# Kernel tuning notes

Hardware: AMD Instinct MI355X
Metric: run time of the kernel (lower is better)

Reference implementation:

```python
import jax, jax.numpy as jnp
import numpy as np
from jax import lax

N_NODES = 10000
IN_DIM = 144
OUT_DIM = 700
THETA_DIM = 256
TOP_K = 5
BN_EPS = 1e-5
LRELU_SLOPE = 0.01


def setup_inputs() -> dict:
    key = jax.random.key(0)
    ks = jax.random.split(key, 5)
    return {
        "H": jax.random.normal(ks[0], (N_NODES, IN_DIM), dtype=jnp.float32),
        "bn_gamma": jnp.ones((IN_DIM,), jnp.float32),
        "bn_beta": jnp.zeros((IN_DIM,), jnp.float32),
        "W_theta": jax.random.normal(ks[1], (IN_DIM, THETA_DIM), jnp.float32) * (1.0 / np.sqrt(IN_DIM)),
        "b_theta": jax.random.normal(ks[2], (THETA_DIM,), jnp.float32) * 0.01,
        "W_out": jax.random.normal(ks[3], (IN_DIM, OUT_DIM), jnp.float32) * (1.0 / np.sqrt(IN_DIM)),
        "b_out": jax.random.normal(ks[4], (OUT_DIM,), jnp.float32) * 0.01,
    }


def _forward(H, bn_gamma, bn_beta, W_theta, b_theta, W_out, b_out):
    # BatchNorm1d over nodes (training-mode batch statistics, biased variance)
    mean = H.mean(axis=0)
    var = ((H - mean) ** 2).mean(axis=0)
    Hn = (H - mean) * lax.rsqrt(var + BN_EPS) * bn_gamma + bn_beta

    # theta projection -> SAM (spectral angle) adjacency; torch code detaches here
    Hx = Hn @ W_theta + b_theta                                  # [n, 256]
    Xn = Hx / jnp.maximum(jnp.linalg.norm(Hx, axis=1, keepdims=True), 1e-12)
    cos = jnp.clip(Xn @ Xn.T, -1.0, 1.0)                         # [n, n]
    sam = jnp.nan_to_num(jnp.arccos(cos))
    A = jnp.clip(jax.nn.sigmoid(jnp.exp(-0.2 * sam)), 0.1, None)
    A = lax.stop_gradient(A)  # SAM() goes through .detach() in torch

    # per-row top-k=5 mask (argsort(-A) first k columns)
    _, idx = lax.top_k(A, TOP_K)                                  # [n, k]
    n = A.shape[0]
    mask = jnp.zeros_like(A).at[jnp.arange(n)[:, None], idx].set(1.0)
    A = A * mask

    # symmetric normalization D^-0.5 A D^-0.5 (diagonal mm as row/col scaling)
    d = A.sum(axis=1) ** -0.5                                     # [n]
    A_hat = A * d[:, None] * d[None, :]

    out = A_hat @ (Hn @ W_out + b_out)                            # [n, out_dim]
    out = jnp.where(out >= 0, out, LRELU_SLOPE * out)             # LeakyReLU
    return out, A


def reference(H, bn_gamma, bn_beta, W_theta, b_theta, W_out, b_out):
    return _forward(H, bn_gamma, bn_beta, W_theta, b_theta, W_out, b_out)
```

## Files before the change

### kernel.cpp

```cpp
#include <hip/hip_runtime.h>
#include <hip/hip_bf16.h>
#include <math.h>

#define N_NODES 10000
#define NPAD2   10240
#define IN_DIM  144
#define TD      256
#define OD      700
#define TOPK    5
#define GK      160
#define GLD     168
#define LDT     72

typedef __attribute__((ext_vector_type(8))) short short8v;
typedef __attribute__((ext_vector_type(4))) float f32x4;

__device__ inline unsigned short f32_to_bf16_rne(float f){
    unsigned int u = __float_as_uint(f);
    unsigned int r = u + 0x7fffu + ((u >> 16) & 1u);
    return (unsigned short)(r >> 16);
}

__global__ void bn_partial(const float* __restrict__ H, double* __restrict__ part){
    int c = threadIdx.x;
    int b = blockIdx.x;
    if (c >= IN_DIM) return;
    int r0 = b * 80;
    double s = 0.0, q = 0.0;
    #pragma unroll 4
    for (int r = r0; r < r0 + 80; ++r){
        double v = (double)H[r*IN_DIM + c];
        s += v; q += v*v;
    }
    part[b*288 + c]       = s;
    part[b*288 + 144 + c] = q;
}

__global__ void bn_finish(const double* __restrict__ part, double* __restrict__ stats){
    int c = threadIdx.x;
    if (c >= 288) return;
    double s = 0.0;
    for (int b = 0; b < 125; ++b) s += part[b*288 + c];
    stats[c] = s;
}

__global__ __launch_bounds__(256) void theta_kernel(
    const float* __restrict__ H, const float* __restrict__ gam, const float* __restrict__ bet,
    const float* __restrict__ Wt, const float* __restrict__ bt, const double* __restrict__ stats,
    const float* __restrict__ Wo, unsigned short* __restrict__ WoT16,
    float* __restrict__ Xn32, unsigned short* __restrict__ Xh, unsigned short* __restrict__ Hn16)
{
    __shared__ double hn[4][IN_DIM];
    __shared__ double red[4][4];
    __shared__ double invs[4];
    int tid = threadIdx.x;
    int r0 = blockIdx.x * 4;

    if (blockIdx.x < 704 && tid < GK){
        int jj = blockIdx.x;
        float v = (jj < OD && tid < IN_DIM) ? Wo[tid*OD + jj] : 0.0f;
        WoT16[(size_t)jj*GK + tid] = f32_to_bf16_rne(v);
    }

    if (tid < GK){
        int c = tid;
        bool real = (c < IN_DIM);
        double mean = 0.0, scale = 0.0, bb = 0.0;
        if (real){
            mean  = stats[c] * (1.0/10000.0);
            double var = stats[144+c] * (1.0/10000.0) - mean*mean;
            scale = (1.0/sqrt(var + 1e-5)) * (double)gam[c];
            bb    = (double)bet[c];
        }
        for (int r = 0; r < 4; ++r){
            int row = r0 + r;
            float vf = 0.0f;
            if (real && row < N_NODES)
                vf = (float)(((double)H[row*IN_DIM + c] - mean)*scale + bb);
            if (row < 10048) Hn16[(size_t)row*GK + c] = f32_to_bf16_rne(vf);
            if (real) hn[r][c] = (double)vf;
        }
    }
    __syncthreads();

    int j = tid;
    double a0,a1,a2,a3;
    a0=a1=a2=a3=(double)bt[j];
    for (int k = 0; k < IN_DIM; ++k){
        double w = (double)Wt[k*TD + j];
        a0 += hn[0][k]*w; a1 += hn[1][k]*w; a2 += hn[2][k]*w; a3 += hn[3][k]*w;
    }
    float hx0=(float)a0, hx1=(float)a1, hx2=(float)a2, hx3=(float)a3;
    double n0=(double)hx0*(double)hx0, n1=(double)hx1*(double)hx1,
           n2=(double)hx2*(double)hx2, n3=(double)hx3*(double)hx3;
    #pragma unroll
    for (int off=32; off>0; off>>=1){
        n0 += __shfl_down(n0, off);
        n1 += __shfl_down(n1, off);
        n2 += __shfl_down(n2, off);
        n3 += __shfl_down(n3, off);
    }
    int lane = tid & 63, wave = tid >> 6;
    if (lane == 0){ red[0][wave]=n0; red[1][wave]=n1; red[2][wave]=n2; red[3][wave]=n3; }
    __syncthreads();
    if (tid < 4){
        double s = red[tid][0]+red[tid][1]+red[tid][2]+red[tid][3];
        invs[tid] = 1.0 / fmax(sqrt(s), 1e-12);
    }
    __syncthreads();

    float hx[4] = {hx0,hx1,hx2,hx3};
    #pragma unroll
    for (int r = 0; r < 4; ++r){
        int row = r0 + r;
        float xn = 0.0f;
        if (row < N_NODES) xn = (float)((double)hx[r]*invs[r]);
        Xn32[(size_t)row*TD + j] = xn;
        Xh  [(size_t)row*TD + j] = f32_to_bf16_rne(xn);
    }
}

__global__ __launch_bounds__(256,2) void gproj(const unsigned short* __restrict__ Hn16,
    const unsigned short* __restrict__ WoT16, const float* __restrict__ bo,
    float* __restrict__ G)
{
    __shared__ short Al[64*GLD];
    __shared__ short Wl[2][64*GLD];
    int tid = threadIdx.x;
    int w = tid >> 6, lane = tid & 63;
    int l15 = lane & 15, l4 = lane >> 4;
    int i0 = blockIdx.x * 64;

    int sr = tid >> 2, sc = tid & 3;
    #pragma unroll
    for (int p = 0; p < 5; ++p){
        int cb = sc + (p<<2);
        *(short8v*)(&Al[sr*GLD + cb*8]) =
            *(const short8v*)(&Hn16[(size_t)(i0+sr)*GK + cb*8]);
    }
    #pragma unroll
    for (int p = 0; p < 5; ++p){
        int cb = sc + (p<<2);
        *(short8v*)(&Wl[0][sr*GLD + cb*8]) =
            *(const short8v*)(&WoT16[(size_t)sr*GK + cb*8]);
    }
    __syncthreads();

    for (int jt = 0; jt < 11; ++jt){
        int cur = jt & 1;
        bool pf = (jt < 10);
        short8v g[5];
        if (pf){
            #pragma unroll
            for (int p = 0; p < 5; ++p){
                int cb = sc + (p<<2);
                g[p] = *(const short8v*)(&WoT16[(size_t)((jt+1)*64 + sr)*GK + cb*8]);
            }
        }
        f32x4 acc[4];
        #pragma unroll
        for (int n=0;n<4;++n) acc[n] = (f32x4){0.f,0.f,0.f,0.f};
        #pragma unroll
        for (int ks = 0; ks < 5; ++ks){
            short8v af = *(const short8v*)(&Al[(w*16 + l15)*GLD + ks*32 + l4*8]);
            #pragma unroll
            for (int n=0;n<4;++n){
                short8v bf = *(const short8v*)(&Wl[cur][(n*16 + l15)*GLD + ks*32 + l4*8]);
                acc[n] = __builtin_amdgcn_mfma_f32_16x16x32_bf16(af, bf, acc[n], 0, 0, 0);
            }
        }
        #pragma unroll
        for (int n=0;n<4;++n){
            int jcol = jt*64 + n*16 + l15;
            if (jcol < OD){
                float b = bo[jcol];
                #pragma unroll
                for (int q=0;q<4;++q){
                    int irow = i0 + w*16 + l4*4 + q;
                    if (irow < N_NODES)
                        G[(size_t)irow*OD + jcol] = acc[n][q] + b;
                }
            }
        }
        if (pf){
            #pragma unroll
            for (int p = 0; p < 5; ++p){
                int cb = sc + (p<<2);
                *(short8v*)(&Wl[cur^1][sr*GLD + cb*8]) = g[p];
            }
        }
        __syncthreads();
    }
}

__global__ __launch_bounds__(256,3) void cos_blk(const unsigned short* __restrict__ Xh,
                                                 unsigned int* __restrict__ pkey)
{
    __shared__ unsigned int smem[10240];
    short* Al = (short*)smem;
    short* Bl = ((short*)smem) + 128*LDT;

    int t = blockIdx.x;
    int bi = 0, rem = t;
    while (rem >= 80 - bi){ rem -= 80 - bi; ++bi; }
    int bj = bi + rem;
    int i0 = bi * 128;
    int j0 = bj * 128;

    int tid = threadIdx.x;
    int w = tid >> 6, lane = tid & 63;
    int l15 = lane & 15, l4 = lane >> 4;

    f32x4 acc[2][8];
    #pragma unroll
    for (int jf=0;jf<2;++jf){
        #pragma unroll
        for (int f=0;f<8;++f) acc[jf][f] = (f32x4){0.f,0.f,0.f,0.f};
    }

    int str = tid >> 3;
    int scb = tid & 7;

    for (int kc = 0; kc < TD; kc += 64){
        __syncthreads();
        #pragma unroll
        for (int p=0;p<4;++p){
            int r = p*32 + str;
            *(short8v*)(&Al[r*LDT + scb*8]) =
                *(const short8v*)(&Xh[(size_t)(i0+r)*TD + kc + scb*8]);
            *(short8v*)(&Bl[r*LDT + scb*8]) =
                *(const short8v*)(&Xh[(size_t)(j0+r)*TD + kc + scb*8]);
        }
        __syncthreads();
        #pragma unroll
        for (int ks=0; ks<2; ++ks){
            short8v af0 = *(const short8v*)(&Bl[(w*32 +  0 + l15)*LDT + ks*32 + l4*8]);
            short8v af1 = *(const short8v*)(&Bl[(w*32 + 16 + l15)*LDT + ks*32 + l4*8]);
            #pragma unroll
            for (int f=0; f<8; ++f){
                short8v bf = *(const short8v*)(&Al[(f*16 + l15)*LDT + ks*32 + l4*8]);
                acc[0][f] = __builtin_amdgcn_mfma_f32_16x16x32_bf16(af0, bf, acc[0][f], 0,0,0);
                acc[1][f] = __builtin_amdgcn_mfma_f32_16x16x32_bf16(af1, bf, acc[1][f], 0,0,0);
            }
        }
    }
    __syncthreads();

    unsigned int* lists = smem;

    #pragma unroll
    for (int f=0; f<8; ++f){
        unsigned int t5[5] = {0u,0u,0u,0u,0u};
        #pragma unroll
        for (int jf=0; jf<2; ++jf){
            #pragma unroll
            for (int q=0; q<4; ++q){
                float v = acc[jf][f][q];
                int jl = w*32 + jf*16 + l4*4 + q;
                unsigned int u = __float_as_uint(v);
                unsigned int key = ((int)u < 0) ? ~u : (u | 0x80000000u);
                unsigned int pk = (key & 0xFFFFFF80u) | (unsigned int)(127 - jl);
                if (pk > t5[4]){
                    t5[4] = pk;
                    #pragma unroll
                    for (int s=4;s>0;--s){
                        if (t5[s] > t5[s-1]){ unsigned int tp=t5[s]; t5[s]=t5[s-1]; t5[s-1]=tp; }
                    }
                }
            }
        }
        int row  = f*16 + l15;
        int base = row*80 + (w*4 + l4)*5;
        #pragma unroll
        for (int s=0;s<5;++s) lists[base+s] = t5[s];
    }
    __syncthreads();

    if (tid < 128){
        unsigned int b5[5] = {0u,0u,0u,0u,0u};
        int rb = tid*80;
        for (int c=0;c<80;++c){
            unsigned int pk = lists[rb + c];
            if (pk > b5[4]){
                b5[4] = pk;
                #pragma unroll
                for (int s=4;s>0;--s){
                    if (b5[s] > b5[s-1]){ unsigned int tp=b5[s]; b5[s]=b5[s-1]; b5[s-1]=tp; }
                }
            }
        }
        size_t gb = (size_t)(i0 + tid)*400 + (size_t)bj*5;
        #pragma unroll
        for (int s=0;s<5;++s) pkey[gb + s] = b5[s];
    }

    if (bi == bj) return;

    __syncthreads();

    #pragma unroll
    for (int jf=0; jf<2; ++jf){
        #pragma unroll
        for (int q=0; q<4; ++q){
            unsigned int t5[5] = {0u,0u,0u,0u,0u};
            #pragma unroll
            for (int f=0; f<8; ++f){
                float v = acc[jf][f][q];
                int il = f*16 + l15;
                unsigned int u = __float_as_uint(v);
                unsigned int key = ((int)u < 0) ? ~u : (u | 0x80000000u);
                unsigned int pk = (key & 0xFFFFFF80u) | (unsigned int)(127 - il);
                if (pk > t5[4]){
                    t5[4] = pk;
                    #pragma unroll
                    for (int s=4;s>0;--s){
                        if (t5[s] > t5[s-1]){ unsigned int tp=t5[s]; t5[s]=t5[s-1]; t5[s-1]=tp; }
                    }
                }
            }
            int jl   = w*32 + jf*16 + l4*4 + q;
            int base = jl*80 + l15*5;
            #pragma unroll
            for (int s=0;s<5;++s) lists[base+s] = t5[s];
        }
    }
    __syncthreads();

    if (tid < 128){
        unsigned int b5[5] = {0u,0u,0u,0u,0u};
        int rb = tid*80;
        for (int c=0;c<80;++c){
            unsigned int pk = lists[rb + c];
            if (pk > b5[4]){
                b5[4] = pk;
                #pragma unroll
                for (int s=4;s>0;--s){
                    if (b5[s] > b5[s-1]){ unsigned int tp=b5[s]; b5[s]=b5[s-1]; b5[s-1]=tp; }
                }
            }
        }
        size_t gb = (size_t)(j0 + tid)*400 + (size_t)bi*5;
        #pragma unroll
        for (int s=0;s<5;++s) pkey[gb + s] = b5[s];
    }
}

__global__ __launch_bounds__(64) void select_topk(const unsigned int* __restrict__ pkey,
    const float* __restrict__ Xn32, float* __restrict__ topA, int* __restrict__ topI,
    float* __restrict__ dinv)
{
    __shared__ unsigned int sk[400];
    __shared__ float xi[TD];
    __shared__ int cand[16];
    int row = blockIdx.x, l = threadIdx.x;
    const unsigned int* pr = &pkey[(size_t)row*400];
    for (int t = l; t < 400; t += 64) sk[t] = pr[t];
    for (int k = l; k < TD; k += 64) xi[k] = Xn32[(size_t)row*TD + k];
    __syncthreads();

    for (int s=0; s<16; ++s){
        unsigned int bk = 0u; int bj = 0x7fffffff; int bslot = -1;
        for (int t = l; t < 400; t += 64){
            unsigned int k = sk[t];
            int gj = (t/5)*128 + 127 - (int)(k & 127u);
            if (k > bk || (k == bk && gj < bj)){ bk = k; bj = gj; bslot = t; }
        }
        unsigned int v = bk; int ix = bj;
        #pragma unroll
        for (int off=32; off>0; off>>=1){
            unsigned int ov = (unsigned int)__shfl_xor((int)v, off);
            int oj = __shfl_xor(ix, off);
            if (ov > v || (ov == v && oj < ix)){ v = ov; ix = oj; }
        }
        if (l == 0) cand[s] = ix;
        if (bk == v && bj == ix && bslot >= 0) sk[bslot] = 0u;
        __syncthreads();
    }

    int c = l >> 2, p = l & 3;
    int j  = cand[c];
    int jc = j < N_NODES ? j : 0;
    const float* xj = &Xn32[(size_t)jc*TD + p*64];
    const float* xr = &xi[p*64];
    double s = 0.0;
    for (int k = 0; k < 64; k += 4){
        float4 b = *(const float4*)(&xj[k]);
        float4 a = *(const float4*)(&xr[k]);
        s += (double)a.x*(double)b.x;
        s += (double)a.y*(double)b.y;
        s += (double)a.z*(double)b.z;
        s += (double)a.w*(double)b.w;
    }
    s += __shfl_xor(s, 1);
    s += __shfl_xor(s, 2);

    float cos32 = (float)s;
    cos32 = fminf(fmaxf(cos32, -1.0f), 1.0f);
    float sam = acosf(cos32);
    float e   = expf(-0.2f*sam);
    float key = 1.0f/(1.0f + expf(-e));
    if (j >= N_NODES) key = -1.0f;

    double dsum = 0.0;
    for (int t = 0; t < TOPK; ++t){
        float v = key; int ix = j;
        #pragma unroll
        for (int off=32; off>0; off>>=1){
            float ov = __shfl_xor(v, off);
            int oix  = __shfl_xor(ix, off);
            if (ov > v || (ov == v && oix < ix)){ v = ov; ix = oix; }
        }
        dsum += (double)v;
        if (l == 0){ topA[row*TOPK + t] = v; topI[row*TOPK + t] = ix; }
        if (j == ix) key = -1.0f;
    }
    if (l == 0) dinv[row] = (float)(1.0/sqrt(dsum));
}

__global__ __launch_bounds__(256) void finalize(const float* __restrict__ G,
    const float* __restrict__ topA, const int* __restrict__ topI,
    const float* __restrict__ dinv, float* __restrict__ out, float* __restrict__ Aout)
{
    __shared__ float w[TOPK];
    __shared__ int   jj[TOPK];
    __shared__ float av[TOPK];
    int row = blockIdx.x, tid = threadIdx.x;
    if (tid < TOPK){
        int j = topI[row*TOPK + tid];
        float a = topA[row*TOPK + tid];
        jj[tid] = j;
        av[tid] = a;
        w[tid]  = a * dinv[row] * dinv[j];
    }
    __syncthreads();

    float4* rowp = (float4*)(Aout + (size_t)row*N_NODES);
    const float4 z = {0.f,0.f,0.f,0.f};
    #pragma unroll
    for (int p = 0; p < 10; ++p){
        int c = p*256 + tid;
        if (c < 2500) rowp[c] = z;
    }

    for (int col = tid; col < OD; col += 256){
        float acc = 0.f;
        #pragma unroll
        for (int m=0;m<TOPK;++m) acc = fmaf(w[m], G[(size_t)jj[m]*OD + col], acc);
        out[(size_t)row*OD + col] = acc >= 0.f ? acc : 0.01f*acc;
    }

    __syncthreads();
    if (tid < TOPK)
        Aout[(size_t)row*N_NODES + jj[tid]] = av[tid];
}

__global__ __launch_bounds__(256) void outk(const float* __restrict__ G,
    const float* __restrict__ topA, const int* __restrict__ topI,
    const float* __restrict__ dinv, float* __restrict__ out)
{
    __shared__ float w[TOPK];
    __shared__ int   jj[TOPK];
    int row = blockIdx.x, tid = threadIdx.x;
    if (tid < TOPK){
        int j = topI[row*TOPK + tid];
        jj[tid] = j;
        w[tid]  = topA[row*TOPK + tid] * dinv[row] * dinv[j];
    }
    __syncthreads();
    for (int col = tid; col < OD; col += 256){
        float acc = 0.f;
        #pragma unroll
        for (int m=0;m<TOPK;++m) acc = fmaf(w[m], G[(size_t)jj[m]*OD + col], acc);
        out[(size_t)row*OD + col] = acc >= 0.f ? acc : 0.01f*acc;
    }
}

__global__ __launch_bounds__(256) void zero_scatter(const float* __restrict__ topA,
    const int* __restrict__ topI, float* __restrict__ Aout)
{
    int row = blockIdx.x;
    float4* rowp = (float4*)(Aout + (size_t)row*N_NODES);
    const float4 z = {0.f,0.f,0.f,0.f};
    int tid = threadIdx.x;
    #pragma unroll
    for (int p = 0; p < 10; ++p){
        int c = p*256 + tid;
        if (c < 2500) rowp[c] = z;
    }
    __syncthreads();
    if (tid < TOPK)
        Aout[(size_t)row*N_NODES + topI[row*TOPK + tid]] = topA[row*TOPK + tid];
}

extern "C" void kernel_launch(void* const* d_in, const int* in_sizes, int n_in,
                              void* d_out, int out_size, void* d_ws, size_t ws_size,
                              hipStream_t stream)
{
    const float* H   = (const float*)d_in[0];
    const float* gam = (const float*)d_in[1];
    const float* bet = (const float*)d_in[2];
    const float* Wt  = (const float*)d_in[3];
    const float* bt  = (const float*)d_in[4];
    const float* Wo  = (const float*)d_in[5];
    const float* bo  = (const float*)d_in[6];

    float* out  = (float*)d_out;
    float* Aout = out + (size_t)N_NODES*OD;

    float*          Xn32  = Aout;
    unsigned short* Xh    = (unsigned short*)(Aout + 2621440);
    unsigned short* Hn16  = (unsigned short*)(Aout + 3932160);
    unsigned short* WoT16 = (unsigned short*)(Aout + 4736000);
    float*          G_A   = Aout + 4792320;
    unsigned int*   pkey  = (unsigned int*)(Aout + 11792320);
    double*         bn_part = (double*)(Aout + 15888320);

    double* bn_stats = (double*)d_ws;
    float*  topA  = (float*)d_ws + 576;
    int*    topI  = (int*)((float*)d_ws + 50576);
    float*  dinvp = (float*)d_ws + 100576;
    float*  G_ws  = (float*)d_ws + 110576;

    const size_t wsNeed = (size_t)(110576 + 7000000) * 4;
    const bool gInWs = (ws_size >= wsNeed);
    float* G = gInWs ? G_ws : G_A;

    bn_partial  <<<125, 192, 0, stream>>>(H, bn_part);
    bn_finish   <<<1, 320, 0, stream>>>(bn_part, bn_stats);
    theta_kernel<<<NPAD2/4, 256, 0, stream>>>(H, gam, bet, Wt, bt, bn_stats, Wo, WoT16,
                                              Xn32, Xh, Hn16);
    gproj       <<<157, 256, 0, stream>>>(Hn16, WoT16, bo, G);
    cos_blk     <<<3240, 256, 0, stream>>>(Xh, pkey);
    select_topk <<<N_NODES, 64, 0, stream>>>(pkey, Xn32, topA, topI, dinvp);
    if (gInWs){
        finalize    <<<N_NODES, 256, 0, stream>>>(G, topA, topI, dinvp, out, Aout);
    } else {
        outk        <<<N_NODES, 256, 0, stream>>>(G, topA, topI, dinvp, out);
        zero_scatter<<<N_NODES, 256, 0, stream>>>(topA, topI, Aout);
    }
}
```

Before: 399.2 us.

## Overlap A-matrix zeroing with cosine GEMM and register-prefetch next K chunk

The cos_blk grid gains one extra block per six GEMM tiles. These extra blocks zero the tail of the dense A output, the region beyond where the earlier scratch buffers live, so that memory-bound work runs alongside the compute-bound cosine GEMM. finalize and zero_scatter now only zero the first 1600 rows. The GEMM loop also prefetches the next 64-wide K chunk into registers while the MFMAs run on the current chunk, cutting one barrier per iteration. The cost is extra register pressure and an ordering dependence: select_topk must read pkey before it is overwritten, and the zero range has to match the scratch layout exactly.

```diff
diff --git a/kernel.cpp b/kernel.cpp
--- a/kernel.cpp
+++ b/kernel.cpp
@@ -11,6 +11,10 @@
 #define GK      160
 #define GLD     168
 #define LDT     72
+
+#define ZOFF   15960320u
+#define Z4TOT  21009920u
+#define Z4PB   38908u
 
 typedef __attribute__((ext_vector_type(8))) short short8v;
 typedef __attribute__((ext_vector_type(4))) float f32x4;
@@ -194,13 +198,27 @@
 }
 
 __global__ __launch_bounds__(256,3) void cos_blk(const unsigned short* __restrict__ Xh,
-                                                 unsigned int* __restrict__ pkey)
+                                                 unsigned int* __restrict__ pkey,
+                                                 float4* __restrict__ zb)
 {
     __shared__ unsigned int smem[10240];
+
+    int bid = blockIdx.x;
+    int grp = bid / 7, ph = bid % 7;
+    if (ph == 6){
+        const float4 z = {0.f,0.f,0.f,0.f};
+        size_t base = (size_t)grp * Z4PB;
+        for (unsigned int i = threadIdx.x; i < Z4PB; i += 256){
+            size_t idx = base + i;
+            if (idx < Z4TOT) zb[idx] = z;
+        }
+        return;
+    }
+
     short* Al = (short*)smem;
     short* Bl = ((short*)smem) + 128*LDT;
 
-    int t = blockIdx.x;
+    int t = grp*6 + ph;
     int bi = 0, rem = t;
     while (rem >= 80 - bi){ rem -= 80 - bi; ++bi; }
     int bj = bi + rem;
@@ -221,17 +239,34 @@
     int str = tid >> 3;
     int scb = tid & 7;
 
-    for (int kc = 0; kc < TD; kc += 64){
-        __syncthreads();
+    {
+        short8v ga[4], gb[4];
         #pragma unroll
         for (int p=0;p<4;++p){
             int r = p*32 + str;
-            *(short8v*)(&Al[r*LDT + scb*8]) =
-                *(const short8v*)(&Xh[(size_t)(i0+r)*TD + kc + scb*8]);
-            *(short8v*)(&Bl[r*LDT + scb*8]) =
-                *(const short8v*)(&Xh[(size_t)(j0+r)*TD + kc + scb*8]);
-        }
-        __syncthreads();
+            ga[p] = *(const short8v*)(&Xh[(size_t)(i0+r)*TD + scb*8]);
+            gb[p] = *(const short8v*)(&Xh[(size_t)(j0+r)*TD + scb*8]);
+        }
+        #pragma unroll
+        for (int p=0;p<4;++p){
+            int r = p*32 + str;
+            *(short8v*)(&Al[r*LDT + scb*8]) = ga[p];
+            *(short8v*)(&Bl[r*LDT + scb*8]) = gb[p];
+        }
+    }
+    __syncthreads();
+
+    for (int kc = 0; kc < 4; ++kc){
+        short8v na[4], nb[4];
+        if (kc < 3){
+            int kn = (kc+1)*64;
+            #pragma unroll
+            for (int p=0;p<4;++p){
+                int r = p*32 + str;
+                na[p] = *(const short8v*)(&Xh[(size_t)(i0+r)*TD + kn + scb*8]);
+                nb[p] = *(const short8v*)(&Xh[(size_t)(j0+r)*TD + kn + scb*8]);
+            }
+        }
         #pragma unroll
         for (int ks=0; ks<2; ++ks){
             short8v af0 = *(const short8v*)(&Bl[(w*32 +  0 + l15)*LDT + ks*32 + l4*8]);
@@ -242,6 +277,16 @@
                 acc[0][f] = __builtin_amdgcn_mfma_f32_16x16x32_bf16(af0, bf, acc[0][f], 0,0,0);
                 acc[1][f] = __builtin_amdgcn_mfma_f32_16x16x32_bf16(af1, bf, acc[1][f], 0,0,0);
             }
+        }
+        __syncthreads();
+        if (kc < 3){
+            #pragma unroll
+            for (int p=0;p<4;++p){
+                int r = p*32 + str;
+                *(short8v*)(&Al[r*LDT + scb*8]) = na[p];
+                *(short8v*)(&Bl[r*LDT + scb*8]) = nb[p];
+            }
+            __syncthreads();
         }
     }
     __syncthreads();
@@ -434,12 +479,14 @@
     }
     __syncthreads();
 
-    float4* rowp = (float4*)(Aout + (size_t)row*N_NODES);
-    const float4 z = {0.f,0.f,0.f,0.f};
-    #pragma unroll
-    for (int p = 0; p < 10; ++p){
-        int c = p*256 + tid;
-        if (c < 2500) rowp[c] = z;
+    if (row < 1600){
+        float4* rowp = (float4*)(Aout + (size_t)row*N_NODES);
+        const float4 z = {0.f,0.f,0.f,0.f};
+        #pragma unroll
+        for (int p = 0; p < 10; ++p){
+            int c = p*256 + tid;
+            if (c < 2500) rowp[c] = z;
+        }
     }
 
     for (int col = tid; col < OD; col += 256){
@@ -479,13 +526,15 @@
     const int* __restrict__ topI, float* __restrict__ Aout)
 {
     int row = blockIdx.x;
-    float4* rowp = (float4*)(Aout + (size_t)row*N_NODES);
-    const float4 z = {0.f,0.f,0.f,0.f};
     int tid = threadIdx.x;
-    #pragma unroll
-    for (int p = 0; p < 10; ++p){
-        int c = p*256 + tid;
-        if (c < 2500) rowp[c] = z;
+    if (row < 1600){
+        float4* rowp = (float4*)(Aout + (size_t)row*N_NODES);
+        const float4 z = {0.f,0.f,0.f,0.f};
+        #pragma unroll
+        for (int p = 0; p < 10; ++p){
+            int c = p*256 + tid;
+            if (c < 2500) rowp[c] = z;
+        }
     }
     __syncthreads();
     if (tid < TOPK)
@@ -525,12 +574,14 @@
     const bool gInWs = (ws_size >= wsNeed);
     float* G = gInWs ? G_ws : G_A;
 
+    float4* zb = (float4*)(Aout + ZOFF);
+
     bn_partial  <<<125, 192, 0, stream>>>(H, bn_part);
     bn_finish   <<<1, 320, 0, stream>>>(bn_part, bn_stats);
     theta_kernel<<<NPAD2/4, 256, 0, stream>>>(H, gam, bet, Wt, bt, bn_stats, Wo, WoT16,
                                               Xn32, Xh, Hn16);
     gproj       <<<157, 256, 0, stream>>>(Hn16, WoT16, bo, G);
-    cos_blk     <<<3240, 256, 0, stream>>>(Xh, pkey);
+    cos_blk     <<<3780, 256, 0, stream>>>(Xh, pkey, zb);
     select_topk <<<N_NODES, 64, 0, stream>>>(pkey, Xn32, topA, topI, dinvp);
     if (gInWs){
         finalize    <<<N_NODES, 256, 0, stream>>>(G, topA, topI, dinvp, out, Aout);
```

Result: faster. 353.4 us (-11.5%).
